# Kernel tuning notes

Hardware: AMD Instinct MI355X
Metric: run time of the kernel (lower is better)

Reference implementation:

```python
import jax, jax.numpy as jnp
import numpy as np

DT = 0.002  # hardcoded dt0 in SDE.__call__
B, T, D = 4096, 2500, 3


def setup_inputs() -> dict:
    key = jax.random.key(0)
    ks = jax.random.split(key, 6)
    # drift/diffusion scaled by 0.1 so 2500-step Euler paths stay numerically stable in fp32
    return {
        "x0": jax.random.normal(ks[0], (B, D), jnp.float32),
        "drift": jax.random.normal(ks[1], (D, D), jnp.float32) * 0.1,
        "drift_bias": jax.random.normal(ks[2], (D,), jnp.float32),
        "diffusion": jax.random.normal(ks[3], (D, D), jnp.float32) * 0.1,
        "diffusion_bias": jax.random.normal(ks[4], (D,), jnp.float32) * 0.1,
        # standard-normal Brownian increments (scaled by sqrt(dt) inside reference)
        "noise": jax.random.normal(ks[5], (T, B, D), jnp.float32),
    }


def reference(x0, drift, drift_bias, diffusion, diffusion_bias, noise):
    # Euler-Maruyama: x_{k+1} = x_k + (A x_k + b) dt + diag(C x_k + d) dW_k
    # (diag(v) @ dW == v * dW elementwise), vmapped over batch via broadcasting.
    dt = jnp.asarray(DT, x0.dtype)
    sqrt_dt = jnp.sqrt(dt)

    def step(x, eps):
        dW = sqrt_dt * eps                       # [B, D]
        x_new = x + (x @ drift.T + drift_bias) * dt \
                + (x @ diffusion.T + diffusion_bias) * dW
        return x_new, x_new

    _, ys = jax.lax.scan(step, x0, noise)        # ys: [T, B, D]
    paths = jnp.concatenate([x0[None], ys], axis=0)  # [T+1, B, D], SaveAt includes t0
    return jnp.transpose(paths, (1, 0, 2))       # [B, T+1, D] like vmapped sol.ys
```

## Files before the change

### kernel.cpp

```cpp
#include <hip/hip_runtime.h>
#include <math.h>
#include <type_traits>


constexpr int B_N  = 4096;
constexpr int T_N  = 2500;
constexpr int CL   = 48;
constexpr int NFC  = T_N / CL;
constexpr int TAIL = T_N - NFC*CL;
constexpr int NCH  = NFC + 1;
constexpr int FLP  = 12;
constexpr int FL   = 16;
constexpr int ROWF = (T_N + 1) * 3;

template <int N> using ic = std::integral_constant<int, N>;


__global__ __launch_bounds__(64)
void sde_chunk_transforms(const float* __restrict__ A,
                          const float* __restrict__ bv,
                          const float* __restrict__ C,
                          const float* __restrict__ dv,
                          const float* __restrict__ noise,
                          float* __restrict__ trans)
{
    const int b = blockIdx.x * 64 + threadIdx.x;
    const int c = blockIdx.y;

    const float dt  = 0.002f;
    const float sdt = sqrtf(dt);

    float IA[3][3], Cs[3][3], bdt[3], ds[3];
#pragma unroll
    for (int i = 0; i < 3; ++i) {
        bdt[i] = bv[i] * dt;
        ds[i]  = dv[i] * sdt;
#pragma unroll
        for (int j = 0; j < 3; ++j) {
            IA[i][j] = A[i * 3 + j] * dt + (i == j ? 1.0f : 0.0f);
            Cs[i][j] = C[i * 3 + j] * sdt;
        }
    }

    float M[3][3] = {{1,0,0},{0,1,0},{0,0,1}};
    float v[3] = {0, 0, 0};

    const float* __restrict__ nb = noise + (size_t)c * CL * (B_N * 3) + (size_t)b * 3;
    const size_t nstride = (size_t)B_N * 3;

    float bufA[FLP][3], bufB[FLP][3];

    auto loadChunk = [&](float (&buf)[FLP][3], int s) {
#pragma unroll
        for (int k = 0; k < FLP; ++k) {
            const float* p = nb + ((size_t)s * FLP + k) * nstride;
            buf[k][0] = p[0];
            buf[k][1] = p[1];
            buf[k][2] = p[2];
        }
    };

    auto compChunk = [&](const float (&buf)[FLP][3]) {
#pragma unroll
        for (int k = 0; k < FLP; ++k) {
            const float e[3] = { buf[k][0], buf[k][1], buf[k][2] };
            float S[3][3], t[3];
#pragma unroll
            for (int i = 0; i < 3; ++i) {
                t[i] = fmaf(e[i], ds[i], bdt[i]);
#pragma unroll
                for (int j = 0; j < 3; ++j)
                    S[i][j] = fmaf(e[i], Cs[i][j], IA[i][j]);
            }
            float nM[3][3], nv[3];
#pragma unroll
            for (int i = 0; i < 3; ++i) {
#pragma unroll
                for (int j = 0; j < 3; ++j)
                    nM[i][j] = fmaf(S[i][2], M[2][j], fmaf(S[i][1], M[1][j], S[i][0] * M[0][j]));
                nv[i] = fmaf(S[i][2], v[2], fmaf(S[i][1], v[1], S[i][0] * v[0])) + t[i];
            }
#pragma unroll
            for (int i = 0; i < 3; ++i) {
                v[i] = nv[i];
#pragma unroll
                for (int j = 0; j < 3; ++j) M[i][j] = nM[i][j];
            }
        }
    };

    loadChunk(bufA, 0);
    loadChunk(bufB, 1);
    compChunk(bufA);
    loadChunk(bufA, 2);
    compChunk(bufB);
    loadChunk(bufB, 3);
    compChunk(bufA);
    compChunk(bufB);

    float* tp = trans + ((size_t)c * B_N + b) * 12;
    float4 w0 = { M[0][0], M[0][1], M[0][2], M[1][0] };
    float4 w1 = { M[1][1], M[1][2], M[2][0], M[2][1] };
    float4 w2 = { M[2][2], v[0],    v[1],    v[2]    };
    ((float4*)tp)[0] = w0;
    ((float4*)tp)[1] = w1;
    ((float4*)tp)[2] = w2;
}

__global__ __launch_bounds__(64)
void sde_scan(const float* __restrict__ x0,
              float* __restrict__ trans)
{
    const int b = blockIdx.x * 64 + threadIdx.x;

    float x[3] = { x0[b * 3 + 0], x0[b * 3 + 1], x0[b * 3 + 2] };

    float4* tp0 = (float4*)(trans + (size_t)b * 12);
    const size_t cstride4 = (size_t)B_N * 3;

    float4 a0 = tp0[0], a1 = tp0[1], a2 = tp0[2];

    for (int c = 0; c < NFC; ++c) {
        float4 b0, b1, b2;
        if (c + 1 < NFC) {
            const float4* tn = tp0 + (size_t)(c + 1) * cstride4;
            b0 = tn[0]; b1 = tn[1]; b2 = tn[2];
        }

        tp0[(size_t)c * cstride4] = make_float4(x[0], x[1], x[2], 0.0f);

        const float n0 = fmaf(a0.x, x[0], fmaf(a0.y, x[1], fmaf(a0.z, x[2], a2.y)));
        const float n1 = fmaf(a0.w, x[0], fmaf(a1.x, x[1], fmaf(a1.y, x[2], a2.z)));
        const float n2 = fmaf(a1.z, x[0], fmaf(a1.w, x[1], fmaf(a2.x, x[2], a2.w)));
        x[0] = n0; x[1] = n1; x[2] = n2;

        a0 = b0; a1 = b1; a2 = b2;
    }

    tp0[(size_t)NFC * cstride4] = make_float4(x[0], x[1], x[2], 0.0f);
}

__global__ __launch_bounds__(256)
void sde_replay(const float* __restrict__ A,
                const float* __restrict__ bv,
                const float* __restrict__ C,
                const float* __restrict__ dv,
                const float* __restrict__ noise,
                const float* __restrict__ trans,
                float* __restrict__ out)
{
    __shared__ float lds[4][FL * 3][66];

    const int widx = threadIdx.x >> 6;
    const int lane = threadIdx.x & 63;
    const int wg   = blockIdx.x * 4 + widx;
    const int pg   = wg & 63;
    const int c    = wg >> 6;
    const int b    = (pg << 6) | lane;

    const float dt  = 0.002f;
    const float sdt = sqrtf(dt);

    float Adt[3][3], Cs[3][3], bdt[3], dsv[3];
#pragma unroll
    for (int i = 0; i < 3; ++i) {
        bdt[i] = bv[i] * dt;
        dsv[i] = dv[i] * sdt;
#pragma unroll
        for (int j = 0; j < 3; ++j) {
            Adt[i][j] = A[i * 3 + j] * dt;
            Cs[i][j]  = C[i * 3 + j] * sdt;
        }
    }

    const float4 xb = *(const float4*)(trans + ((size_t)c * B_N + b) * 12);
    float x0r = xb.x, x1r = xb.y, x2r = xb.z;

    const float* __restrict__ nb = noise + (size_t)c * CL * (B_N * 3) + (size_t)b * 3;
    const size_t nstride = (size_t)B_N * 3;

    auto stepf = [&](float e0, float e1, float e2) {
        const float a0 = fmaf(Adt[0][2], x2r, fmaf(Adt[0][1], x1r, fmaf(Adt[0][0], x0r, bdt[0])));
        const float a1 = fmaf(Adt[1][2], x2r, fmaf(Adt[1][1], x1r, fmaf(Adt[1][0], x0r, bdt[1])));
        const float a2 = fmaf(Adt[2][2], x2r, fmaf(Adt[2][1], x1r, fmaf(Adt[2][0], x0r, bdt[2])));

        const float c0 = fmaf(Cs[0][2], x2r, fmaf(Cs[0][1], x1r, fmaf(Cs[0][0], x0r, dsv[0])));
        const float c1 = fmaf(Cs[1][2], x2r, fmaf(Cs[1][1], x1r, fmaf(Cs[1][0], x0r, dsv[1])));
        const float c2 = fmaf(Cs[2][2], x2r, fmaf(Cs[2][1], x1r, fmaf(Cs[2][0], x0r, dsv[2])));

        x0r = fmaf(c0, e0, x0r + a0);
        x1r = fmaf(c1, e1, x1r + a1);
        x2r = fmaf(c2, e2, x2r + a2);
    };

    if (c == NFC) {
        float* op = out + (size_t)b * ROWF + (size_t)NFC * CL * 3;
        op[0] = x0r; op[1] = x1r; op[2] = x2r; op += 3;
#pragma unroll
        for (int k = 0; k < TAIL; ++k) {
            const float* p = nb + (size_t)k * nstride;
            stepf(p[0], p[1], p[2]);
            op[0] = x0r; op[1] = x1r; op[2] = x2r; op += 3;
        }
        return;
    }

    float (*tile)[66] = lds[widx];

    const int h = lane >> 4;
    const int m = lane & 15;
    float* const outbase = out + (size_t)(pg << 6) * ROWF + (size_t)c * (CL * 3);

    auto writeState = [&](int k) {
        tile[3 * k + 0][lane] = x0r;
        tile[3 * k + 1][lane] = x1r;
        tile[3 * k + 2][lane] = x2r;
    };

    auto warGuard = [&]() {
        asm volatile("s_waitcnt lgkmcnt(0)" ::: "memory");
        __builtin_amdgcn_sched_barrier(0);
    };

    auto storeFlush = [&](int f) {
        asm volatile("s_waitcnt lgkmcnt(0)" ::: "memory");
        __builtin_amdgcn_sched_barrier(0);
#pragma unroll
        for (int i = 0; i < 16; ++i) {
            const int p = i * 4 + h;
            const float v0 = tile[3 * m + 0][p];
            const float v1 = tile[3 * m + 1][p];
            const float v2 = tile[3 * m + 2][p];
            float* dst = outbase + (size_t)p * ROWF + f * (FL * 3) + m * 3;
            dst[0] = v0; dst[1] = v1; dst[2] = v2;
        }
    };

    float bufA[FL][3], bufB[FL][3];

    auto loadN = [&](float (&buf)[FL][3], int base, auto cntc) {
        constexpr int CNT = decltype(cntc)::value;
#pragma unroll
        for (int k = 0; k < CNT; ++k) {
            const float* p = nb + (size_t)(base + k) * nstride;
            buf[k][0] = p[0];
            buf[k][1] = p[1];
            buf[k][2] = p[2];
        }
    };

    loadN(bufA, 0,  ic<15>{});
    loadN(bufB, 15, ic<16>{});

    writeState(0);
#pragma unroll
    for (int k = 0; k < 15; ++k) {
        stepf(bufA[k][0], bufA[k][1], bufA[k][2]);
        writeState(k + 1);
    }
    loadN(bufA, 31, ic<16>{});
    storeFlush(0);

    warGuard();
#pragma unroll
    for (int k = 0; k < 16; ++k) {
        stepf(bufB[k][0], bufB[k][1], bufB[k][2]);
        writeState(k);
    }
    storeFlush(1);

    warGuard();
#pragma unroll
    for (int k = 0; k < 16; ++k) {
        stepf(bufA[k][0], bufA[k][1], bufA[k][2]);
        writeState(k);
    }
    storeFlush(2);
}

extern "C" void kernel_launch(void* const* d_in, const int* in_sizes, int n_in,
                              void* d_out, int out_size, void* d_ws, size_t ws_size,
                              hipStream_t stream) {
    const float* x0    = (const float*)d_in[0];
    const float* A     = (const float*)d_in[1];
    const float* bv    = (const float*)d_in[2];
    const float* C     = (const float*)d_in[3];
    const float* dv    = (const float*)d_in[4];
    const float* noise = (const float*)d_in[5];
    float* out = (float*)d_out;

    float* trans = (float*)d_ws;

    dim3 gridPC(B_N / 64, NFC);

    sde_chunk_transforms<<<gridPC, 64, 0, stream>>>(A, bv, C, dv, noise, trans);
    sde_scan<<<B_N / 64, 64, 0, stream>>>(x0, trans);
    sde_replay<<<(B_N / 64) * NCH / 4, 256, 0, stream>>>(A, bv, C, dv, noise, trans, out);
}
```

Measured before the change: 90.91 us.

## Stagger per-lane output phases in replay and prefetch scan transforms four deep

The replay kernel now runs one 64-thread wave per block. Each lane gets a per-lane phase offset into a 32-row circular LDS tile, so the transposed global stores of different lanes fall on staggered positions. Chunk 0 writes its first phi states directly and the last chunk masks its tail, which changes the store addressing and boundary handling. The scan kernel now keeps four chunk transforms in flight in rotating registers instead of one, to hide global load latency on its serial chain. The aim is to improve store coalescing and bank or channel distribution and to reduce latency stalls, at the cost of more complex indexing, extra boundary branches, and overlapping recompute at chunk edges.

```diff
diff --git a/kernel.cpp b/kernel.cpp
--- a/kernel.cpp
+++ b/kernel.cpp
@@ -7,10 +7,8 @@
 constexpr int T_N  = 2500;
 constexpr int CL   = 48;
 constexpr int NFC  = T_N / CL;
-constexpr int TAIL = T_N - NFC*CL;
 constexpr int NCH  = NFC + 1;
 constexpr int FLP  = 12;
-constexpr int FL   = 16;
 constexpr int ROWF = (T_N + 1) * 3;
 
 template <int N> using ic = std::integral_constant<int, N>;
@@ -116,31 +114,43 @@
     float x[3] = { x0[b * 3 + 0], x0[b * 3 + 1], x0[b * 3 + 2] };
 
     float4* tp0 = (float4*)(trans + (size_t)b * 12);
-    const size_t cstride4 = (size_t)B_N * 3;
-
-    float4 a0 = tp0[0], a1 = tp0[1], a2 = tp0[2];
-
-    for (int c = 0; c < NFC; ++c) {
-        float4 b0, b1, b2;
-        if (c + 1 < NFC) {
-            const float4* tn = tp0 + (size_t)(c + 1) * cstride4;
-            b0 = tn[0]; b1 = tn[1]; b2 = tn[2];
-        }
-
-        tp0[(size_t)c * cstride4] = make_float4(x[0], x[1], x[2], 0.0f);
-
+    const size_t cs = (size_t)B_N * 3;
+
+    float4 qa0, qa1, qa2, qb0, qb1, qb2, qc0, qc1, qc2, qd0, qd1, qd2;
+
+    auto L = [&](int s, float4& r0, float4& r1, float4& r2) {
+        const float4* tn = tp0 + (size_t)s * cs;
+        r0 = tn[0]; r1 = tn[1]; r2 = tn[2];
+    };
+    auto useSlot = [&](int s, const float4& a0, const float4& a1, const float4& a2) {
+        tp0[(size_t)s * cs] = make_float4(x[0], x[1], x[2], 0.0f);
         const float n0 = fmaf(a0.x, x[0], fmaf(a0.y, x[1], fmaf(a0.z, x[2], a2.y)));
         const float n1 = fmaf(a0.w, x[0], fmaf(a1.x, x[1], fmaf(a1.y, x[2], a2.z)));
         const float n2 = fmaf(a1.z, x[0], fmaf(a1.w, x[1], fmaf(a2.x, x[2], a2.w)));
         x[0] = n0; x[1] = n1; x[2] = n2;
-
-        a0 = b0; a1 = b1; a2 = b2;
-    }
-
-    tp0[(size_t)NFC * cstride4] = make_float4(x[0], x[1], x[2], 0.0f);
+    };
+
+    L(0, qa0, qa1, qa2);
+    L(1, qb0, qb1, qb2);
+    L(2, qc0, qc1, qc2);
+    L(3, qd0, qd1, qd2);
+
+    for (int it = 0; it < NFC / 4; ++it) {
+        const int s = it * 4;
+        useSlot(s + 0, qa0, qa1, qa2);
+        if (s + 4 < NFC) L(s + 4, qa0, qa1, qa2);
+        useSlot(s + 1, qb0, qb1, qb2);
+        if (s + 5 < NFC) L(s + 5, qb0, qb1, qb2);
+        useSlot(s + 2, qc0, qc1, qc2);
+        if (s + 6 < NFC) L(s + 6, qc0, qc1, qc2);
+        useSlot(s + 3, qd0, qd1, qd2);
+        if (s + 7 < NFC) L(s + 7, qd0, qd1, qd2);
+    }
+
+    tp0[(size_t)NFC * cs] = make_float4(x[0], x[1], x[2], 0.0f);
 }
 
-__global__ __launch_bounds__(256)
+__global__ __launch_bounds__(64)
 void sde_replay(const float* __restrict__ A,
                 const float* __restrict__ bv,
                 const float* __restrict__ C,
@@ -149,14 +159,13 @@
                 const float* __restrict__ trans,
                 float* __restrict__ out)
 {
-    __shared__ float lds[4][FL * 3][66];
-
-    const int widx = threadIdx.x >> 6;
+    __shared__ float tile[96][66];
+
     const int lane = threadIdx.x & 63;
-    const int wg   = blockIdx.x * 4 + widx;
-    const int pg   = wg & 63;
-    const int c    = wg >> 6;
+    const int pg   = blockIdx.x & 63;
+    const int c    = blockIdx.x >> 6;
     const int b    = (pg << 6) | lane;
+    const int phi  = (11 * lane) & 15;
 
     const float dt  = 0.002f;
     const float sdt = sqrtf(dt);
@@ -176,8 +185,9 @@
     const float4 xb = *(const float4*)(trans + ((size_t)c * B_N + b) * 12);
     float x0r = xb.x, x1r = xb.y, x2r = xb.z;
 
-    const float* __restrict__ nb = noise + (size_t)c * CL * (B_N * 3) + (size_t)b * 3;
+    const float* __restrict__ nb0 = noise + (size_t)b * 3;
     const size_t nstride = (size_t)B_N * 3;
+    const int base48 = c * CL;
 
     auto stepf = [&](float e0, float e1, float e2) {
         const float a0 = fmaf(Adt[0][2], x2r, fmaf(Adt[0][1], x1r, fmaf(Adt[0][0], x0r, bdt[0])));
@@ -194,88 +204,130 @@
     };
 
     if (c == NFC) {
-        float* op = out + (size_t)b * ROWF + (size_t)NFC * CL * 3;
-        op[0] = x0r; op[1] = x1r; op[2] = x2r; op += 3;
-#pragma unroll
-        for (int k = 0; k < TAIL; ++k) {
-            const float* p = nb + (size_t)k * nstride;
+        float* op = out + (size_t)b * ROWF;
+        if (phi == 0) {
+            op[2496 * 3 + 0] = x0r; op[2496 * 3 + 1] = x1r; op[2496 * 3 + 2] = x2r;
+        }
+#pragma unroll
+        for (int k = 0; k < 4; ++k) {
+            const float* p = nb0 + (size_t)(2496 + k) * nstride;
             stepf(p[0], p[1], p[2]);
-            op[0] = x0r; op[1] = x1r; op[2] = x2r; op += 3;
+            const int j = k + 1;
+            if (j >= phi) {
+                float* d = op + (size_t)(2496 + j) * 3;
+                d[0] = x0r; d[1] = x1r; d[2] = x2r;
+            }
         }
         return;
     }
 
-    float (*tile)[66] = lds[widx];
-
-    const int h = lane >> 4;
-    const int m = lane & 15;
-    float* const outbase = out + (size_t)(pg << 6) * ROWF + (size_t)c * (CL * 3);
-
-    auto writeState = [&](int k) {
-        tile[3 * k + 0][lane] = x0r;
-        tile[3 * k + 1][lane] = x1r;
-        tile[3 * k + 2][lane] = x2r;
-    };
-
+    const bool c0   = (c == 0);
+    const bool last = (c == NFC - 1);
+
+    auto tileWrite = [&](int j) {
+        const int r = (j & 31) * 3;
+        tile[r + 0][lane] = x0r;
+        tile[r + 1][lane] = x1r;
+        tile[r + 2][lane] = x2r;
+    };
+
+    auto rawGuard = [&]() {
+        asm volatile("s_waitcnt lgkmcnt(0)" ::: "memory");
+        __builtin_amdgcn_sched_barrier(0);
+    };
     auto warGuard = [&]() {
         asm volatile("s_waitcnt lgkmcnt(0)" ::: "memory");
         __builtin_amdgcn_sched_barrier(0);
     };
 
-    auto storeFlush = [&](int f) {
-        asm volatile("s_waitcnt lgkmcnt(0)" ::: "memory");
-        __builtin_amdgcn_sched_barrier(0);
+    const int h   = lane >> 4;
+    const int m   = lane & 15;
+    const int phh = (11 * h) & 15;
+    float* const outG = out + (size_t)(pg << 6) * ROWF + (size_t)base48 * 3;
+
+    auto flush = [&](auto fc, bool maskTail) {
+        constexpr int F = decltype(fc)::value;
+        rawGuard();
 #pragma unroll
         for (int i = 0; i < 16; ++i) {
-            const int p = i * 4 + h;
-            const float v0 = tile[3 * m + 0][p];
-            const float v1 = tile[3 * m + 1][p];
-            const float v2 = tile[3 * m + 2][p];
-            float* dst = outbase + (size_t)p * ROWF + f * (FL * 3) + m * 3;
-            dst[0] = v0; dst[1] = v1; dst[2] = v2;
-        }
-    };
-
-    float bufA[FL][3], bufB[FL][3];
-
-    auto loadN = [&](float (&buf)[FL][3], int base, auto cntc) {
-        constexpr int CNT = decltype(cntc)::value;
+            const int P    = 4 * i + h;
+            const int phiP = (12 * i + phh) & 15;
+            const int j    = phiP + 16 * F + m;
+            const int r    = (j & 31) * 3;
+            const float v0 = tile[r + 0][P];
+            const float v1 = tile[r + 1][P];
+            const float v2 = tile[r + 2][P];
+            if (!maskTail || (phiP + m) <= 20) {
+                float* d = outG + (size_t)P * ROWF + (size_t)j * 3;
+                d[0] = v0; d[1] = v1; d[2] = v2;
+            }
+        }
+    };
+
+    float bufA[16][3], bufB[16][3];
+    auto loadN = [&](float (&buf)[16][3], int kbase, auto cnt) {
+        constexpr int CNT = decltype(cnt)::value;
 #pragma unroll
         for (int k = 0; k < CNT; ++k) {
-            const float* p = nb + (size_t)(base + k) * nstride;
+            int g = base48 + kbase + k;
+            g = g > (T_N - 1) ? (T_N - 1) : g;
+            const float* p = nb0 + (size_t)g * nstride;
             buf[k][0] = p[0];
             buf[k][1] = p[1];
             buf[k][2] = p[2];
         }
     };
 
-    loadN(bufA, 0,  ic<15>{});
-    loadN(bufB, 15, ic<16>{});
-
-    writeState(0);
+    loadN(bufA, 0,  ic<16>{});
+    loadN(bufB, 16, ic<16>{});
+
+    tileWrite(0);
+    if (c0 && phi > 0) {
+        float* d = outG + (size_t)lane * ROWF;
+        d[0] = x0r; d[1] = x1r; d[2] = x2r;
+    }
+
+#pragma unroll
+    for (int k = 0; k < 16; ++k) {
+        stepf(bufA[k][0], bufA[k][1], bufA[k][2]);
+        tileWrite(k + 1);
+        if (c0 && (k + 1) < phi) {
+            float* d = outG + (size_t)lane * ROWF + (size_t)(k + 1) * 3;
+            d[0] = x0r; d[1] = x1r; d[2] = x2r;
+        }
+    }
+    loadN(bufA, 32, ic<16>{});
+
+#pragma unroll
+    for (int k = 0; k < 15; ++k) {
+        stepf(bufB[k][0], bufB[k][1], bufB[k][2]);
+        tileWrite(k + 17);
+    }
+    loadN(bufB, 48, ic<14>{});
+
+    flush(ic<0>{}, false);
+
+    warGuard();
+    stepf(bufB[15][0], bufB[15][1], bufB[15][2]);
+    tileWrite(32);
 #pragma unroll
     for (int k = 0; k < 15; ++k) {
         stepf(bufA[k][0], bufA[k][1], bufA[k][2]);
-        writeState(k + 1);
-    }
-    loadN(bufA, 31, ic<16>{});
-    storeFlush(0);
+        tileWrite(33 + k);
+    }
+
+    flush(ic<1>{}, false);
 
     warGuard();
-#pragma unroll
-    for (int k = 0; k < 16; ++k) {
+    stepf(bufA[15][0], bufA[15][1], bufA[15][2]);
+    tileWrite(48);
+#pragma unroll
+    for (int k = 0; k < 14; ++k) {
         stepf(bufB[k][0], bufB[k][1], bufB[k][2]);
-        writeState(k);
-    }
-    storeFlush(1);
-
-    warGuard();
-#pragma unroll
-    for (int k = 0; k < 16; ++k) {
-        stepf(bufA[k][0], bufA[k][1], bufA[k][2]);
-        writeState(k);
-    }
-    storeFlush(2);
+        tileWrite(49 + k);
+    }
+
+    flush(ic<2>{}, last);
 }
 
 extern "C" void kernel_launch(void* const* d_in, const int* in_sizes, int n_in,
@@ -295,5 +347,5 @@
 
     sde_chunk_transforms<<<gridPC, 64, 0, stream>>>(A, bv, C, dv, noise, trans);
     sde_scan<<<B_N / 64, 64, 0, stream>>>(x0, trans);
-    sde_replay<<<(B_N / 64) * NCH / 4, 256, 0, stream>>>(A, bv, C, dv, noise, trans, out);
+    sde_replay<<<64 * NCH, 64, 0, stream>>>(A, bv, C, dv, noise, trans, out);
 }
```

New measurement: 83.11 us. -8.6%, faster.
